# Optimization experiments

Measured on AMD Instinct MI355X. Metric: run time of the kernel, lower is better.

## Reference

```python
import jax, jax.numpy as jnp
import numpy as np

DIM, HEADS, DHEAD = 256, 8, 64
HID = HEADS * DHEAD


def _elu1(x):
    # F.elu(x) + 1 == exp(x) for x<0, x+1 for x>=0
    return jnp.where(x > 0, x + 1.0, jnp.exp(x))


def setup_inputs() -> dict:
    key = jax.random.key(0)
    ks = jax.random.split(key, 6)
    B, H, W = 8, 64, 64
    x = jax.random.normal(ks[0], (B, DIM, H, W), dtype=jnp.float32)
    contact_map = jax.random.uniform(ks[1], (B, 1, H, W), dtype=jnp.float32)
    s_qkv = 1.0 / np.sqrt(DIM)
    Wqkv = jax.random.normal(ks[2], (3 * HID, DIM), dtype=jnp.float32) * s_qkv
    s_out = 1.0 / np.sqrt(HID)
    Wout = jax.random.normal(ks[3], (DIM, HID), dtype=jnp.float32) * s_out
    bout = jax.random.normal(ks[4], (DIM,), dtype=jnp.float32) * 0.01
    contact_scale = jnp.float32(0.1)
    return {"x": x, "contact_map": contact_map, "Wqkv": Wqkv,
            "Wout": Wout, "bout": bout, "contact_scale": contact_scale}


def reference(x, contact_map, Wqkv, Wout, bout, contact_scale):
    b, c, h, w = x.shape
    n = h * w
    xf = x.reshape(b, c, n)                                  # b c n
    qkv = jnp.einsum('oc,bcn->bon', Wqkv, xf)                # b (3*H*D) n
    qkv = qkv.reshape(b, 3, HEADS, DHEAD, n)                 # qkv-major channel order
    q = _elu1(qkv[:, 0])                                     # b h d n
    k = _elu1(qkv[:, 1])
    v = qkv[:, 2]
    cm = contact_map.reshape(b, 1, 1, n)                     # b 1 1 n
    k = k * (1.0 + contact_scale * cm)
    kv = jnp.einsum('bhdn,bhen->bhde', k, v)                 # b h d e
    ksum = k.sum(axis=-1)                                    # b h d
    z = 1.0 / (jnp.einsum('bhdn,bhd->bhn', q, ksum) + 1e-6)  # b h n
    out = jnp.einsum('bhde,bhdn->bhne', kv, q) * z[..., None]  # b h n e
    out = out.transpose(0, 1, 3, 2).reshape(b, HID, n)       # b (h d) n
    y = jnp.einsum('oc,bcn->bon', Wout, out) + bout[None, :, None]
    return y.reshape(b, -1, h, w)
```

## Files before the change

### kernel.cpp

```cpp
#include <hip/hip_runtime.h>
#include <stdint.h>


#define NPIX 4096
#define HIDC 512
#define DIMC 256
#define BATCH 8

typedef __attribute__((ext_vector_type(8))) short bf16x8;
typedef __attribute__((ext_vector_type(4))) float f32x4;

__device__ __forceinline__ float bf2f(unsigned short h) {
    unsigned int u = ((unsigned int)h) << 16; float f;
    __builtin_memcpy(&f, &u, 4); return f;
}
__device__ __forceinline__ unsigned short f2bf(float f) {
    unsigned int u; __builtin_memcpy(&u, &f, 4);
    u += 0x7fffu + ((u >> 16) & 1u);
    return (unsigned short)(u >> 16);
}
__device__ __forceinline__ float elu1(float x) {
    return x > 0.f ? x + 1.f : __expf(x);
}

__global__ __launch_bounds__(256) void k_convW(
    const float* __restrict__ Wqkv, const float* __restrict__ Wout,
    unsigned short* __restrict__ Wb, unsigned short* __restrict__ Wob)
{
    int i4 = (blockIdx.x * 256 + threadIdx.x) * 4;
    const int NW1 = 1536 * 256;
    float4 v; unsigned short* dst;
    if (i4 < NW1) { v = *(const float4*)&Wqkv[i4]; dst = Wb + i4; }
    else { int j = i4 - NW1; v = *(const float4*)&Wout[j]; dst = Wob + j; }
    ushort4 o; o.x = f2bf(v.x); o.y = f2bf(v.y); o.z = f2bf(v.z); o.w = f2bf(v.w);
    *(ushort4*)dst = o;
}

__global__ __launch_bounds__(256) void k_tx(
    const float* __restrict__ x, unsigned short* __restrict__ xT)
{
    __shared__ float tile[32][33];
    const int n0 = blockIdx.x * 32, c0 = blockIdx.y * 32, b = blockIdx.z;
    const int t = threadIdx.x;
    const int r = t >> 3, c4 = (t & 7) * 4;
    float4 v = *(const float4*)&x[((size_t)b * DIMC + c0 + r) * NPIX + n0 + c4];
    tile[r][c4 + 0] = v.x; tile[r][c4 + 1] = v.y;
    tile[r][c4 + 2] = v.z; tile[r][c4 + 3] = v.w;
    __syncthreads();
    ushort4 o;
    unsigned short* op = (unsigned short*)&o;
#pragma unroll
    for (int i = 0; i < 4; i++) op[i] = f2bf(tile[c4 + i][r]);
    *(ushort4*)&xT[((size_t)b * NPIX + n0 + r) * DIMC + c0 + c4] = o;
}

__global__ __launch_bounds__(256) void k_qkv(
    const unsigned short* __restrict__ xT,
    const unsigned short* __restrict__ Wb,
    const float* __restrict__ cmp,
    const float* __restrict__ csp,
    unsigned short* __restrict__ qT,
    unsigned short* __restrict__ kb,
    unsigned short* __restrict__ vb)
{
    const int b  = blockIdx.z;
    const int m0 = blockIdx.x * 128;
    const int n0 = blockIdx.y * 128;
    const int t = threadIdx.x;
    const int wave = t >> 6, lane = t & 63;
    const int wm = wave >> 1, wn = wave & 1;
    const int lrow = lane & 15, quad = lane >> 4;

    __shared__ unsigned short As[128 * 32];
    __shared__ unsigned short Bs[128 * 32];

    const unsigned short* Ag = xT + ((size_t)b * NPIX + m0) * DIMC;
    const unsigned short* Bg = Wb + (size_t)n0 * DIMC;

    f32x4 acc[4][4];
#pragma unroll
    for (int i = 0; i < 4; i++)
#pragma unroll
        for (int j = 0; j < 4; j++) acc[i][j] = (f32x4){0.f, 0.f, 0.f, 0.f};

    for (int k0 = 0; k0 < DIMC; k0 += 32) {
#pragma unroll
        for (int i = 0; i < 2; i++) {
            int chunk = t + i * 256;
            int row = chunk >> 2, c8 = (chunk & 3) * 8;
            *(uint4*)&As[row * 32 + c8] = *(const uint4*)&Ag[(size_t)row * DIMC + k0 + c8];
            *(uint4*)&Bs[row * 32 + c8] = *(const uint4*)&Bg[(size_t)row * DIMC + k0 + c8];
        }
        __syncthreads();
        bf16x8 af[4], bfr[4];
#pragma unroll
        for (int mt = 0; mt < 4; mt++)
            af[mt] = *(const bf16x8*)&As[(wm * 64 + mt * 16 + lrow) * 32 + quad * 8];
#pragma unroll
        for (int nt = 0; nt < 4; nt++)
            bfr[nt] = *(const bf16x8*)&Bs[(wn * 64 + nt * 16 + lrow) * 32 + quad * 8];
#pragma unroll
        for (int mt = 0; mt < 4; mt++)
#pragma unroll
            for (int nt = 0; nt < 4; nt++)
                acc[mt][nt] = __builtin_amdgcn_mfma_f32_16x16x32_bf16(
                    af[mt], bfr[nt], acc[mt][nt], 0, 0, 0);
        __syncthreads();
    }

    const int sect = n0 >> 9;
    const float cs = *csp;

#pragma unroll
    for (int mt = 0; mt < 4; mt++) {
        const int pixel0 = m0 + wm * 64 + mt * 16 + quad * 4;
        float4 cmv;
        if (sect == 1) cmv = *(const float4*)&cmp[(size_t)b * NPIX + pixel0];
        const float* cm4 = (const float*)&cmv;
#pragma unroll
        for (int nt = 0; nt < 4; nt++) {
            const int o = n0 + wn * 64 + nt * 16 + lrow;
            f32x4 a = acc[mt][nt];
            if (sect == 0) {
#pragma unroll
                for (int r = 0; r < 4; r++)
                    qT[((size_t)b * NPIX + pixel0 + r) * HIDC + o] = f2bf(elu1(a[r]));
            } else if (sect == 1) {
                ushort4 st; unsigned short* sp = (unsigned short*)&st;
#pragma unroll
                for (int r = 0; r < 4; r++)
                    sp[r] = f2bf(elu1(a[r]) * (1.f + cs * cm4[r]));
                *(ushort4*)&kb[((size_t)b * HIDC + (o - 512)) * NPIX + pixel0] = st;
            } else {
                ushort4 st; unsigned short* sp = (unsigned short*)&st;
#pragma unroll
                for (int r = 0; r < 4; r++) sp[r] = f2bf(a[r]);
                *(ushort4*)&vb[((size_t)b * HIDC + (o - 1024)) * NPIX + pixel0] = st;
            }
        }
    }
}

__global__ __launch_bounds__(256) void k_kv(
    const unsigned short* __restrict__ kb, const unsigned short* __restrict__ vb,
    float* __restrict__ kv, float* __restrict__ ksum)
{
    const int bh = blockIdx.y, nc = blockIdx.x;
    const int t = threadIdx.x, wave = t >> 6, lane = t & 63;
    const int lrow = lane & 15, quad = lane >> 4;

    __shared__ unsigned short ks[64 * 32];
    __shared__ unsigned short vs[64 * 32];

    const size_t base = (size_t)bh * 64 * NPIX;
    f32x4 acc[4];
#pragma unroll
    for (int i = 0; i < 4; i++) acc[i] = (f32x4){0.f, 0.f, 0.f, 0.f};
    float ksacc = 0.f;

    const int row = t >> 2, c8 = (t & 3) * 8;

    for (int step = 0; step < 16; step++) {
        const int ncol = nc * 512 + step * 32;
        uint4 kq = *(const uint4*)&kb[base + (size_t)row * NPIX + ncol + c8];
        *(uint4*)&ks[row * 32 + c8] = kq;
        *(uint4*)&vs[row * 32 + c8] = *(const uint4*)&vb[base + (size_t)row * NPIX + ncol + c8];
        const unsigned short* kp = (const unsigned short*)&kq;
#pragma unroll
        for (int j = 0; j < 8; j++) ksacc += bf2f(kp[j]);
        __syncthreads();
        bf16x8 bfv = *(const bf16x8*)&vs[(wave * 16 + lrow) * 32 + quad * 8];
#pragma unroll
        for (int mt = 0; mt < 4; mt++) {
            bf16x8 af = *(const bf16x8*)&ks[(mt * 16 + lrow) * 32 + quad * 8];
            acc[mt] = __builtin_amdgcn_mfma_f32_16x16x32_bf16(af, bfv, acc[mt], 0, 0, 0);
        }
        __syncthreads();
    }

    float* kvb = kv + (size_t)bh * 4096;
#pragma unroll
    for (int mt = 0; mt < 4; mt++)
#pragma unroll
        for (int r = 0; r < 4; r++)
            atomicAdd(&kvb[(mt * 16 + quad * 4 + r) * 64 + wave * 16 + lrow], acc[mt][r]);
    atomicAdd(&ksum[bh * 64 + row], ksacc);
}

__global__ __launch_bounds__(256) void k_out(
    const unsigned short* __restrict__ qT,
    const float* __restrict__ kv, const float* __restrict__ ksum,
    unsigned short* __restrict__ outT)
{
    const int bh = blockIdx.y, p0 = blockIdx.x * 128;
    const int b = bh >> 3, h = bh & 7;
    const int t = threadIdx.x, wave = t >> 6, lane = t & 63;
    const int lrow = lane & 15, quad = lane >> 4;

    __shared__ unsigned short Aq[128 * 64];
    __shared__ unsigned short Bv[80 * 64];

    const unsigned short* qg = qT + ((size_t)b * NPIX + p0) * HIDC + h * 64;
#pragma unroll
    for (int i = 0; i < 4; i++) {
        int chunk = t + i * 256;
        int row = chunk >> 3, c8 = (chunk & 7) * 8;
        *(uint4*)&Aq[row * 64 + c8] = *(const uint4*)&qg[(size_t)row * HIDC + c8];
    }
    const float* kvg = kv + (size_t)bh * 4096;
#pragma unroll
    for (int i = 0; i < 16; i++) {
        int idx = t + i * 256;
        int e = idx >> 6, d = idx & 63;
        Bv[e * 64 + d] = f2bf(kvg[(size_t)d * 64 + e]);
    }
    if (t < 64) {
        float ksv = ksum[bh * 64 + t];
        unsigned short hi = f2bf(ksv);
        Bv[64 * 64 + t] = hi;
        Bv[65 * 64 + t] = f2bf(ksv - bf2f(hi));
#pragma unroll
        for (int rr = 66; rr < 80; rr++) Bv[rr * 64 + t] = 0;
    }
    __syncthreads();

    f32x4 acc[2][5];
#pragma unroll
    for (int i = 0; i < 2; i++)
#pragma unroll
        for (int j = 0; j < 5; j++) acc[i][j] = (f32x4){0.f, 0.f, 0.f, 0.f};

#pragma unroll
    for (int ksp = 0; ksp < 2; ksp++) {
        bf16x8 af[2], bfr[5];
#pragma unroll
        for (int mt = 0; mt < 2; mt++)
            af[mt] = *(const bf16x8*)&Aq[(wave * 32 + mt * 16 + lrow) * 64 + ksp * 32 + quad * 8];
#pragma unroll
        for (int nt = 0; nt < 5; nt++)
            bfr[nt] = *(const bf16x8*)&Bv[(nt * 16 + lrow) * 64 + ksp * 32 + quad * 8];
#pragma unroll
        for (int mt = 0; mt < 2; mt++)
#pragma unroll
            for (int nt = 0; nt < 5; nt++)
                acc[mt][nt] = __builtin_amdgcn_mfma_f32_16x16x32_bf16(
                    af[mt], bfr[nt], acc[mt][nt], 0, 0, 0);
    }

    unsigned short* og = outT + ((size_t)b * NPIX + p0) * HIDC + h * 64;
#pragma unroll
    for (int mt = 0; mt < 2; mt++) {
        const int prow = wave * 32 + mt * 16 + quad * 4;
        float z[4];
#pragma unroll
        for (int r = 0; r < 4; r++) {
            float hi = __shfl(acc[mt][4][r], lane & 48);
            float lo = __shfl(acc[mt][4][r], (lane & 48) | 1);
            z[r] = 1.f / (hi + lo + 1e-6f);
        }
#pragma unroll
        for (int nt = 0; nt < 4; nt++)
#pragma unroll
            for (int r = 0; r < 4; r++)
                og[(size_t)(prow + r) * HIDC + nt * 16 + lrow] = f2bf(acc[mt][nt][r] * z[r]);
    }
}

__global__ __launch_bounds__(256) void k_y(
    const unsigned short* __restrict__ outT,
    const unsigned short* __restrict__ Wob,
    const float* __restrict__ bout,
    float* __restrict__ y)
{
    const int b  = blockIdx.z;
    const int m0 = blockIdx.x * 128;
    const int n0 = blockIdx.y * 128;
    const int t = threadIdx.x;
    const int wave = t >> 6, lane = t & 63;
    const int wm = wave >> 1, wn = wave & 1;
    const int lrow = lane & 15, quad = lane >> 4;

    __shared__ unsigned short As[128 * 32];
    __shared__ unsigned short Bs[128 * 32];

    const unsigned short* Ag = outT + ((size_t)b * NPIX + m0) * HIDC;
    const unsigned short* Bg = Wob + (size_t)n0 * HIDC;

    f32x4 acc[4][4];
#pragma unroll
    for (int i = 0; i < 4; i++)
#pragma unroll
        for (int j = 0; j < 4; j++) acc[i][j] = (f32x4){0.f, 0.f, 0.f, 0.f};

    for (int k0 = 0; k0 < HIDC; k0 += 32) {
#pragma unroll
        for (int i = 0; i < 2; i++) {
            int chunk = t + i * 256;
            int row = chunk >> 2, c8 = (chunk & 3) * 8;
            *(uint4*)&As[row * 32 + c8] = *(const uint4*)&Ag[(size_t)row * HIDC + k0 + c8];
            *(uint4*)&Bs[row * 32 + c8] = *(const uint4*)&Bg[(size_t)row * HIDC + k0 + c8];
        }
        __syncthreads();
        bf16x8 af[4], bfr[4];
#pragma unroll
        for (int mt = 0; mt < 4; mt++)
            af[mt] = *(const bf16x8*)&As[(wm * 64 + mt * 16 + lrow) * 32 + quad * 8];
#pragma unroll
        for (int nt = 0; nt < 4; nt++)
            bfr[nt] = *(const bf16x8*)&Bs[(wn * 64 + nt * 16 + lrow) * 32 + quad * 8];
#pragma unroll
        for (int mt = 0; mt < 4; mt++)
#pragma unroll
            for (int nt = 0; nt < 4; nt++)
                acc[mt][nt] = __builtin_amdgcn_mfma_f32_16x16x32_bf16(
                    af[mt], bfr[nt], acc[mt][nt], 0, 0, 0);
        __syncthreads();
    }

#pragma unroll
    for (int mt = 0; mt < 4; mt++) {
        const int pixel0 = m0 + wm * 64 + mt * 16 + quad * 4;
#pragma unroll
        for (int nt = 0; nt < 4; nt++) {
            const int o = n0 + wn * 64 + nt * 16 + lrow;
            const float bias = bout[o];
            f32x4 a = acc[mt][nt];
            float4 st; st.x = a[0] + bias; st.y = a[1] + bias;
            st.z = a[2] + bias; st.w = a[3] + bias;
            *(float4*)&y[((size_t)b * DIMC + o) * NPIX + pixel0] = st;
        }
    }
}

extern "C" void kernel_launch(void* const* d_in, const int* in_sizes, int n_in,
                              void* d_out, int out_size, void* d_ws, size_t ws_size,
                              hipStream_t stream) {
    (void)in_sizes; (void)n_in; (void)out_size; (void)ws_size;
    const float* x    = (const float*)d_in[0];
    const float* cm   = (const float*)d_in[1];
    const float* Wqkv = (const float*)d_in[2];
    const float* Wout = (const float*)d_in[3];
    const float* bout = (const float*)d_in[4];
    const float* csp  = (const float*)d_in[5];
    float* y = (float*)d_out;

    const size_t qn = (size_t)BATCH * HIDC * NPIX;
    char* ws = (char*)d_ws;
    unsigned short* qT   = (unsigned short*)ws;                 ws += qn * 2;
    unsigned short* kb   = (unsigned short*)ws;                 ws += qn * 2;
    unsigned short* vb   = (unsigned short*)ws;                 ws += qn * 2;
    unsigned short* outT = (unsigned short*)ws;                 ws += qn * 2;
    unsigned short* xT   = outT;
    float* kvp   = (float*)ws;                                  ws += (size_t)64 * 64 * 64 * 4;
    float* ksump = (float*)ws;                                  ws += (size_t)64 * 64 * 4;
    unsigned short* Wb  = (unsigned short*)ws;                  ws += (size_t)1536 * 256 * 2;
    unsigned short* Wob = (unsigned short*)ws;

    hipMemsetAsync(kvp, 0, ((size_t)64 * 64 * 64 + 64 * 64) * sizeof(float), stream);
    k_convW<<<512, 256, 0, stream>>>(Wqkv, Wout, Wb, Wob);
    k_tx  <<<dim3(128, 8, 8), 256, 0, stream>>>(x, xT);
    k_qkv <<<dim3(32, 12, 8), 256, 0, stream>>>(xT, Wb, cm, csp, qT, kb, vb);
    k_kv  <<<dim3(8, 64),     256, 0, stream>>>(kb, vb, kvp, ksump);
    k_out <<<dim3(32, 64),    256, 0, stream>>>(qT, kvp, ksump, outT);
    k_y   <<<dim3(32, 2, 8),  256, 0, stream>>>(outT, Wob, bout, y);
}
```

Before: 223.2 us.

## Switch to 32x32 MFMA, pad LDS rows, transpose k/v epilogue operands

The QKV and output-attention kernels move from 16x16x32 to 32x32x16 bf16 MFMA tiles. In the QKV kernel, the k and v sections swap the A and B operands so each lane writes along the pixel dimension of the channel-major k/v buffers. All GEMM-style kernels pad their LDS row stride (to 40 or 72 elements) to cut bank conflicts. The k_out kernel also reads kv contiguously during its transpose into LDS. The larger tiles cut fragment loads per MFMA, at the cost of larger accumulators and scalar 2-byte stores.

After: 214.8 us. 3.8% less time.

```diff
diff --git a/kernel.cpp b/kernel.cpp
--- a/kernel.cpp
+++ b/kernel.cpp
@@ -9,6 +9,7 @@
 
 typedef __attribute__((ext_vector_type(8))) short bf16x8;
 typedef __attribute__((ext_vector_type(4))) float f32x4;
+typedef __attribute__((ext_vector_type(16))) float f32x16;
 
 __device__ __forceinline__ float bf2f(unsigned short h) {
     unsigned int u = ((unsigned int)h) << 16; float f;
@@ -54,6 +55,7 @@
     *(ushort4*)&xT[((size_t)b * NPIX + n0 + r) * DIMC + c0 + c4] = o;
 }
 
+#define LS1 40
 __global__ __launch_bounds__(256) void k_qkv(
     const unsigned short* __restrict__ xT,
     const unsigned short* __restrict__ Wb,
@@ -69,78 +71,94 @@
     const int t = threadIdx.x;
     const int wave = t >> 6, lane = t & 63;
     const int wm = wave >> 1, wn = wave & 1;
-    const int lrow = lane & 15, quad = lane >> 4;
-
-    __shared__ unsigned short As[128 * 32];
-    __shared__ unsigned short Bs[128 * 32];
+    const int l31 = lane & 31, lhi = lane >> 5;
+    const int sect = n0 >> 9;
+
+    __shared__ unsigned short As[128 * LS1];
+    __shared__ unsigned short Bs[128 * LS1];
 
     const unsigned short* Ag = xT + ((size_t)b * NPIX + m0) * DIMC;
     const unsigned short* Bg = Wb + (size_t)n0 * DIMC;
 
-    f32x4 acc[4][4];
-#pragma unroll
-    for (int i = 0; i < 4; i++)
-#pragma unroll
-        for (int j = 0; j < 4; j++) acc[i][j] = (f32x4){0.f, 0.f, 0.f, 0.f};
-
+    const unsigned short* mArr = (sect == 0) ? As : Bs;
+    const unsigned short* nArr = (sect == 0) ? Bs : As;
+
+    f32x16 acc[2][2];
+#pragma unroll
+    for (int i = 0; i < 2; i++)
+#pragma unroll
+        for (int j = 0; j < 2; j++)
+#pragma unroll
+            for (int r = 0; r < 16; r++) acc[i][j][r] = 0.f;
+
+    const int srow = t >> 2, sc8 = (t & 3) * 8;
     for (int k0 = 0; k0 < DIMC; k0 += 32) {
-#pragma unroll
-        for (int i = 0; i < 2; i++) {
-            int chunk = t + i * 256;
-            int row = chunk >> 2, c8 = (chunk & 3) * 8;
-            *(uint4*)&As[row * 32 + c8] = *(const uint4*)&Ag[(size_t)row * DIMC + k0 + c8];
-            *(uint4*)&Bs[row * 32 + c8] = *(const uint4*)&Bg[(size_t)row * DIMC + k0 + c8];
-        }
-        __syncthreads();
-        bf16x8 af[4], bfr[4];
-#pragma unroll
-        for (int mt = 0; mt < 4; mt++)
-            af[mt] = *(const bf16x8*)&As[(wm * 64 + mt * 16 + lrow) * 32 + quad * 8];
-#pragma unroll
-        for (int nt = 0; nt < 4; nt++)
-            bfr[nt] = *(const bf16x8*)&Bs[(wn * 64 + nt * 16 + lrow) * 32 + quad * 8];
-#pragma unroll
-        for (int mt = 0; mt < 4; mt++)
-#pragma unroll
-            for (int nt = 0; nt < 4; nt++)
-                acc[mt][nt] = __builtin_amdgcn_mfma_f32_16x16x32_bf16(
-                    af[mt], bfr[nt], acc[mt][nt], 0, 0, 0);
-        __syncthreads();
-    }
-
-    const int sect = n0 >> 9;
+        *(uint4*)&As[srow * LS1 + sc8] =
+            *(const uint4*)&Ag[(size_t)srow * DIMC + k0 + sc8];
+        *(uint4*)&As[(srow + 64) * LS1 + sc8] =
+            *(const uint4*)&Ag[(size_t)(srow + 64) * DIMC + k0 + sc8];
+        *(uint4*)&Bs[srow * LS1 + sc8] =
+            *(const uint4*)&Bg[(size_t)srow * DIMC + k0 + sc8];
+        *(uint4*)&Bs[(srow + 64) * LS1 + sc8] =
+            *(const uint4*)&Bg[(size_t)(srow + 64) * DIMC + k0 + sc8];
+        __syncthreads();
+#pragma unroll
+        for (int ks = 0; ks < 2; ks++) {
+            bf16x8 af[2], bfg[2];
+#pragma unroll
+            for (int fm = 0; fm < 2; fm++)
+                af[fm] = *(const bf16x8*)&mArr[(wm * 64 + fm * 32 + l31) * LS1 + ks * 16 + lhi * 8];
+#pragma unroll
+            for (int fn = 0; fn < 2; fn++)
+                bfg[fn] = *(const bf16x8*)&nArr[(wn * 64 + fn * 32 + l31) * LS1 + ks * 16 + lhi * 8];
+#pragma unroll
+            for (int fm = 0; fm < 2; fm++)
+#pragma unroll
+                for (int fn = 0; fn < 2; fn++)
+                    acc[fm][fn] = __builtin_amdgcn_mfma_f32_32x32x16_bf16(
+                        af[fm], bfg[fn], acc[fm][fn], 0, 0, 0);
+        }
+        __syncthreads();
+    }
+
     const float cs = *csp;
-
-#pragma unroll
-    for (int mt = 0; mt < 4; mt++) {
-        const int pixel0 = m0 + wm * 64 + mt * 16 + quad * 4;
-        float4 cmv;
-        if (sect == 1) cmv = *(const float4*)&cmp[(size_t)b * NPIX + pixel0];
-        const float* cm4 = (const float*)&cmv;
-#pragma unroll
-        for (int nt = 0; nt < 4; nt++) {
-            const int o = n0 + wn * 64 + nt * 16 + lrow;
-            f32x4 a = acc[mt][nt];
-            if (sect == 0) {
-#pragma unroll
-                for (int r = 0; r < 4; r++)
-                    qT[((size_t)b * NPIX + pixel0 + r) * HIDC + o] = f2bf(elu1(a[r]));
-            } else if (sect == 1) {
-                ushort4 st; unsigned short* sp = (unsigned short*)&st;
-#pragma unroll
-                for (int r = 0; r < 4; r++)
-                    sp[r] = f2bf(elu1(a[r]) * (1.f + cs * cm4[r]));
-                *(ushort4*)&kb[((size_t)b * HIDC + (o - 512)) * NPIX + pixel0] = st;
-            } else {
-                ushort4 st; unsigned short* sp = (unsigned short*)&st;
-#pragma unroll
-                for (int r = 0; r < 4; r++) sp[r] = f2bf(a[r]);
-                *(ushort4*)&vb[((size_t)b * HIDC + (o - 1024)) * NPIX + pixel0] = st;
+    if (sect == 0) {
+#pragma unroll
+        for (int fm = 0; fm < 2; fm++) {
+            const int pbase = m0 + wm * 64 + fm * 32;
+#pragma unroll
+            for (int fn = 0; fn < 2; fn++) {
+                const int o = n0 + wn * 64 + fn * 32 + l31;
+#pragma unroll
+                for (int r = 0; r < 16; r++) {
+                    int prow = pbase + (r & 3) + 8 * (r >> 2) + 4 * lhi;
+                    qT[((size_t)b * NPIX + prow) * HIDC + o] = f2bf(elu1(acc[fm][fn][r]));
+                }
             }
         }
-    }
-}
-
+    } else {
+        unsigned short* dstb = (sect == 1) ? kb : vb;
+#pragma unroll
+        for (int fm = 0; fm < 2; fm++) {
+            const int obase = (n0 & 511) + wm * 64 + fm * 32;
+#pragma unroll
+            for (int fn = 0; fn < 2; fn++) {
+                const int pixel = m0 + wn * 64 + fn * 32 + l31;
+                float g = 1.f;
+                if (sect == 1) g = 1.f + cs * cmp[(size_t)b * NPIX + pixel];
+#pragma unroll
+                for (int r = 0; r < 16; r++) {
+                    int orow = obase + (r & 3) + 8 * (r >> 2) + 4 * lhi;
+                    float val = acc[fm][fn][r];
+                    if (sect == 1) val = elu1(val) * g;
+                    dstb[((size_t)b * HIDC + orow) * NPIX + pixel] = f2bf(val);
+                }
+            }
+        }
+    }
+}
+
+#define LS2 40
 __global__ __launch_bounds__(256) void k_kv(
     const unsigned short* __restrict__ kb, const unsigned short* __restrict__ vb,
     float* __restrict__ kv, float* __restrict__ ksum)
@@ -149,8 +167,8 @@
     const int t = threadIdx.x, wave = t >> 6, lane = t & 63;
     const int lrow = lane & 15, quad = lane >> 4;
 
-    __shared__ unsigned short ks[64 * 32];
-    __shared__ unsigned short vs[64 * 32];
+    __shared__ unsigned short ks[64 * LS2];
+    __shared__ unsigned short vs[64 * LS2];
 
     const size_t base = (size_t)bh * 64 * NPIX;
     f32x4 acc[4];
@@ -163,16 +181,16 @@
     for (int step = 0; step < 16; step++) {
         const int ncol = nc * 512 + step * 32;
         uint4 kq = *(const uint4*)&kb[base + (size_t)row * NPIX + ncol + c8];
-        *(uint4*)&ks[row * 32 + c8] = kq;
-        *(uint4*)&vs[row * 32 + c8] = *(const uint4*)&vb[base + (size_t)row * NPIX + ncol + c8];
+        *(uint4*)&ks[row * LS2 + c8] = kq;
+        *(uint4*)&vs[row * LS2 + c8] = *(const uint4*)&vb[base + (size_t)row * NPIX + ncol + c8];
         const unsigned short* kp = (const unsigned short*)&kq;
 #pragma unroll
         for (int j = 0; j < 8; j++) ksacc += bf2f(kp[j]);
         __syncthreads();
-        bf16x8 bfv = *(const bf16x8*)&vs[(wave * 16 + lrow) * 32 + quad * 8];
+        bf16x8 bfv = *(const bf16x8*)&vs[(wave * 16 + lrow) * LS2 + quad * 8];
 #pragma unroll
         for (int mt = 0; mt < 4; mt++) {
-            bf16x8 af = *(const bf16x8*)&ks[(mt * 16 + lrow) * 32 + quad * 8];
+            bf16x8 af = *(const bf16x8*)&ks[(mt * 16 + lrow) * LS2 + quad * 8];
             acc[mt] = __builtin_amdgcn_mfma_f32_16x16x32_bf16(af, bfv, acc[mt], 0, 0, 0);
         }
         __syncthreads();
@@ -187,6 +205,7 @@
     atomicAdd(&ksum[bh * 64 + row], ksacc);
 }
 
+#define LS3 72
 __global__ __launch_bounds__(256) void k_out(
     const unsigned short* __restrict__ qT,
     const float* __restrict__ kv, const float* __restrict__ ksum,
@@ -195,74 +214,62 @@
     const int bh = blockIdx.y, p0 = blockIdx.x * 128;
     const int b = bh >> 3, h = bh & 7;
     const int t = threadIdx.x, wave = t >> 6, lane = t & 63;
-    const int lrow = lane & 15, quad = lane >> 4;
-
-    __shared__ unsigned short Aq[128 * 64];
-    __shared__ unsigned short Bv[80 * 64];
+    const int l31 = lane & 31, lhi = lane >> 5;
+
+    __shared__ unsigned short Aq[128 * LS3];
+    __shared__ unsigned short Bv[96 * LS3];
 
     const unsigned short* qg = qT + ((size_t)b * NPIX + p0) * HIDC + h * 64;
 #pragma unroll
     for (int i = 0; i < 4; i++) {
-        int chunk = t + i * 256;
-        int row = chunk >> 3, c8 = (chunk & 7) * 8;
-        *(uint4*)&Aq[row * 64 + c8] = *(const uint4*)&qg[(size_t)row * HIDC + c8];
+        int idx = t + i * 256;
+        int row = idx >> 3, c8 = (idx & 7) * 8;
+        *(uint4*)&Aq[row * LS3 + c8] = *(const uint4*)&qg[(size_t)row * HIDC + c8];
     }
     const float* kvg = kv + (size_t)bh * 4096;
 #pragma unroll
     for (int i = 0; i < 16; i++) {
         int idx = t + i * 256;
-        int e = idx >> 6, d = idx & 63;
-        Bv[e * 64 + d] = f2bf(kvg[(size_t)d * 64 + e]);
+        int d = idx >> 6, e = idx & 63;
+        Bv[e * LS3 + d] = f2bf(kvg[idx]);
     }
     if (t < 64) {
         float ksv = ksum[bh * 64 + t];
         unsigned short hi = f2bf(ksv);
-        Bv[64 * 64 + t] = hi;
-        Bv[65 * 64 + t] = f2bf(ksv - bf2f(hi));
-#pragma unroll
-        for (int rr = 66; rr < 80; rr++) Bv[rr * 64 + t] = 0;
-    }
+        Bv[64 * LS3 + t] = hi;
+        Bv[65 * LS3 + t] = f2bf(ksv - bf2f(hi));
+    }
+    for (int i = t; i < 30 * 64; i += 256)
+        Bv[(66 + (i >> 6)) * LS3 + (i & 63)] = 0;
     __syncthreads();
 
-    f32x4 acc[2][5];
-#pragma unroll
-    for (int i = 0; i < 2; i++)
-#pragma unroll
-        for (int j = 0; j < 5; j++) acc[i][j] = (f32x4){0.f, 0.f, 0.f, 0.f};
-
-#pragma unroll
-    for (int ksp = 0; ksp < 2; ksp++) {
-        bf16x8 af[2], bfr[5];
-#pragma unroll
-        for (int mt = 0; mt < 2; mt++)
-            af[mt] = *(const bf16x8*)&Aq[(wave * 32 + mt * 16 + lrow) * 64 + ksp * 32 + quad * 8];
-#pragma unroll
-        for (int nt = 0; nt < 5; nt++)
-            bfr[nt] = *(const bf16x8*)&Bv[(nt * 16 + lrow) * 64 + ksp * 32 + quad * 8];
-#pragma unroll
-        for (int mt = 0; mt < 2; mt++)
-#pragma unroll
-            for (int nt = 0; nt < 5; nt++)
-                acc[mt][nt] = __builtin_amdgcn_mfma_f32_16x16x32_bf16(
-                    af[mt], bfr[nt], acc[mt][nt], 0, 0, 0);
-    }
-
-    unsigned short* og = outT + ((size_t)b * NPIX + p0) * HIDC + h * 64;
-#pragma unroll
-    for (int mt = 0; mt < 2; mt++) {
-        const int prow = wave * 32 + mt * 16 + quad * 4;
-        float z[4];
-#pragma unroll
-        for (int r = 0; r < 4; r++) {
-            float hi = __shfl(acc[mt][4][r], lane & 48);
-            float lo = __shfl(acc[mt][4][r], (lane & 48) | 1);
-            z[r] = 1.f / (hi + lo + 1e-6f);
-        }
-#pragma unroll
-        for (int nt = 0; nt < 4; nt++)
-#pragma unroll
-            for (int r = 0; r < 4; r++)
-                og[(size_t)(prow + r) * HIDC + nt * 16 + lrow] = f2bf(acc[mt][nt][r] * z[r]);
+    f32x16 acc[3];
+#pragma unroll
+    for (int j = 0; j < 3; j++)
+#pragma unroll
+        for (int r = 0; r < 16; r++) acc[j][r] = 0.f;
+
+#pragma unroll
+    for (int ksub = 0; ksub < 4; ksub++) {
+        const int koff = ksub * 16 + lhi * 8;
+        bf16x8 af = *(const bf16x8*)&Aq[(wave * 32 + l31) * LS3 + koff];
+#pragma unroll
+        for (int nf = 0; nf < 3; nf++) {
+            bf16x8 bfg = *(const bf16x8*)&Bv[(nf * 32 + l31) * LS3 + koff];
+            acc[nf] = __builtin_amdgcn_mfma_f32_32x32x16_bf16(af, bfg, acc[nf], 0, 0, 0);
+        }
+    }
+
+    unsigned short* og = outT + ((size_t)b * NPIX + p0 + wave * 32) * HIDC + h * 64;
+#pragma unroll
+    for (int r = 0; r < 16; r++) {
+        float hi = __shfl(acc[2][r], lane & 32);
+        float lo = __shfl(acc[2][r], (lane & 32) | 1);
+        float z = 1.f / (hi + lo + 1e-6f);
+        int prow = (r & 3) + 8 * (r >> 2) + 4 * lhi;
+#pragma unroll
+        for (int nf = 0; nf < 2; nf++)
+            og[(size_t)prow * HIDC + nf * 32 + l31] = f2bf(acc[nf][r] * z);
     }
 }
 
@@ -280,8 +287,8 @@
     const int wm = wave >> 1, wn = wave & 1;
     const int lrow = lane & 15, quad = lane >> 4;
 
-    __shared__ unsigned short As[128 * 32];
-    __shared__ unsigned short Bs[128 * 32];
+    __shared__ unsigned short As[128 * LS1];
+    __shared__ unsigned short Bs[128 * LS1];
 
     const unsigned short* Ag = outT + ((size_t)b * NPIX + m0) * HIDC;
     const unsigned short* Bg = Wob + (size_t)n0 * HIDC;
@@ -292,22 +299,24 @@
 #pragma unroll
         for (int j = 0; j < 4; j++) acc[i][j] = (f32x4){0.f, 0.f, 0.f, 0.f};
 
+    const int srow = t >> 2, sc8 = (t & 3) * 8;
     for (int k0 = 0; k0 < HIDC; k0 += 32) {
-#pragma unroll
-        for (int i = 0; i < 2; i++) {
-            int chunk = t + i * 256;
-            int row = chunk >> 2, c8 = (chunk & 3) * 8;
-            *(uint4*)&As[row * 32 + c8] = *(const uint4*)&Ag[(size_t)row * HIDC + k0 + c8];
-            *(uint4*)&Bs[row * 32 + c8] = *(const uint4*)&Bg[(size_t)row * HIDC + k0 + c8];
-        }
+        *(uint4*)&As[srow * LS1 + sc8] =
+            *(const uint4*)&Ag[(size_t)srow * HIDC + k0 + sc8];
+        *(uint4*)&As[(srow + 64) * LS1 + sc8] =
+            *(const uint4*)&Ag[(size_t)(srow + 64) * HIDC + k0 + sc8];
+        *(uint4*)&Bs[srow * LS1 + sc8] =
+            *(const uint4*)&Bg[(size_t)srow * HIDC + k0 + sc8];
+        *(uint4*)&Bs[(srow + 64) * LS1 + sc8] =
+            *(const uint4*)&Bg[(size_t)(srow + 64) * HIDC + k0 + sc8];
         __syncthreads();
         bf16x8 af[4], bfr[4];
 #pragma unroll
         for (int mt = 0; mt < 4; mt++)
-            af[mt] = *(const bf16x8*)&As[(wm * 64 + mt * 16 + lrow) * 32 + quad * 8];
+            af[mt] = *(const bf16x8*)&As[(wm * 64 + mt * 16 + lrow) * LS1 + quad * 8];
 #pragma unroll
         for (int nt = 0; nt < 4; nt++)
-            bfr[nt] = *(const bf16x8*)&Bs[(wn * 64 + nt * 16 + lrow) * 32 + quad * 8];
+            bfr[nt] = *(const bf16x8*)&Bs[(wn * 64 + nt * 16 + lrow) * LS1 + quad * 8];
 #pragma unroll
         for (int mt = 0; mt < 4; mt++)
 #pragma unroll
```
